# Kernel tuning notes

Measured on AMD Instinct MI355X. Metric: run time of the kernel, lower is better.

Reference implementation:

```python
import jax, jax.numpy as jnp
import numpy as np

RANKS = [16, 16, 16, 16]
ALPHAS = [32.0, 32.0, 32.0, 32.0]
IN_DIM, OUT_DIM = 4096, 4096
BSZ, SEQ = 4, 2048


def _col_scale(dtype):
    # per-column scale alpha_i / rank_i for each adapter's rank block
    s = np.concatenate([np.full(r, a / r, dtype=np.float32) for r, a in zip(RANKS, ALPHAS)])
    return jnp.asarray(s, dtype=dtype)


def setup_inputs() -> dict:
    key = jax.random.key(0)
    k1, k2, k3, k4 = jax.random.split(key, 4)
    total_rank = sum(RANKS)
    x = jax.random.normal(k1, (BSZ, SEQ, IN_DIM), dtype=jnp.float32)
    weight = jax.random.normal(k2, (OUT_DIM, IN_DIM), dtype=jnp.float32) * (1.0 / np.sqrt(IN_DIM))
    lora_a_weight = jax.random.normal(k3, (total_rank, IN_DIM), dtype=jnp.float32) * (1.0 / np.sqrt(IN_DIM))
    lora_b_weight = jax.random.normal(k4, (OUT_DIM, total_rank), dtype=jnp.float32) * 0.02
    return {"x": x, "weight": weight, "lora_a_weight": lora_a_weight, "lora_b_weight": lora_b_weight}


def reference(x, weight, lora_a_weight, lora_b_weight):
    # base: F.linear(x, W) -> x @ W^T        [B,S,out_dim]
    out = jnp.einsum('bsi,oi->bso', x, weight)
    # lora_a: x @ A^T                         [B,S,sum_rank] (dropout p=0 -> no-op)
    lora_a_out = jnp.einsum('bsi,ri->bsr', x, lora_a_weight)
    # The per-adapter masked loop sum_i (alpha_i/r_i) * (lora_a_out * mask_i) @ B^T
    # is mathematically a single GEMM with per-column scaling of lora_a_out.
    scaled = lora_a_out * _col_scale(lora_a_out.dtype)
    lora_out_total = jnp.einsum('bsr,or->bso', scaled, lora_b_weight)
    return out + lora_out_total
```

## Files before the change

kernel.cpp:

```cpp
#include <hip/hip_runtime.h>

typedef __bf16 bf16_t;
typedef __attribute__((ext_vector_type(8))) __bf16 bf16x8;
typedef __attribute__((ext_vector_type(4))) float f32x4;

#define M_DIM 8192
#define N_DIM 4096
#define K_DIM 4096
#define R_DIM 64

__global__ __launch_bounds__(256) void cvt_x(const float* __restrict__ in,
                                             bf16_t* __restrict__ out) {
    size_t i = ((size_t)blockIdx.x * 256 + threadIdx.x) * 8;
    float4 a = *(const float4*)(in + i);
    float4 b = *(const float4*)(in + i + 4);
    bf16x8 v;
    v[0] = (bf16_t)a.x; v[1] = (bf16_t)a.y; v[2] = (bf16_t)a.z; v[3] = (bf16_t)a.w;
    v[4] = (bf16_t)b.x; v[5] = (bf16_t)b.y; v[6] = (bf16_t)b.z; v[7] = (bf16_t)b.w;
    *(bf16x8*)(out + i) = v;
}

__global__ __launch_bounds__(256) void build_weff(const float* __restrict__ W,
                                                  const float* __restrict__ A,
                                                  const float* __restrict__ Bl,
                                                  bf16_t* __restrict__ out) {
    __shared__ __attribute__((aligned(16))) float bls[16 * R_DIM];

    const int i  = blockIdx.x * 256 + threadIdx.x;
    const int o0 = blockIdx.y * 16;

    {
        const int t = threadIdx.x;
        float4 v = *(const float4*)(Bl + o0 * R_DIM + t * 4);
        *(float4*)(bls + t * 4) = v;
    }
    __syncthreads();

    float acc[16];
#pragma unroll
    for (int j = 0; j < 16; j++) acc[j] = W[(size_t)(o0 + j) * K_DIM + i];

    for (int rh = 0; rh < R_DIM; rh += 16) {
        float av[16];
#pragma unroll
        for (int r = 0; r < 16; r++) av[r] = 2.0f * A[(size_t)(rh + r) * K_DIM + i];
#pragma unroll
        for (int j = 0; j < 16; j++) {
#pragma unroll
            for (int rq = 0; rq < 4; rq++) {
                float4 b = *(const float4*)(bls + j * R_DIM + rh + rq * 4);
                acc[j] = fmaf(b.x, av[rq * 4 + 0], acc[j]);
                acc[j] = fmaf(b.y, av[rq * 4 + 1], acc[j]);
                acc[j] = fmaf(b.z, av[rq * 4 + 2], acc[j]);
                acc[j] = fmaf(b.w, av[rq * 4 + 3], acc[j]);
            }
        }
    }
#pragma unroll
    for (int j = 0; j < 16; j++) out[(size_t)(o0 + j) * K_DIM + i] = (bf16_t)acc[j];
}

#define BM 256
#define BN 256
#define BK 64
#define NT (K_DIM / BK)

#define GLDS(gp, lp) __builtin_amdgcn_global_load_lds(                       \
    (__attribute__((address_space(1))) void*)(gp),                           \
    (__attribute__((address_space(3))) void*)(lp), 16, 0, 0)

#define SBAR() __builtin_amdgcn_s_barrier()
#define WAITV(n) asm volatile("s_waitcnt vmcnt(" #n ")" ::: "memory")

#define READ_A(ARR, mbase)                                                   \
    _Pragma("unroll")                                                        \
    for (int mf = 0; mf < 4; ++mf)                                           \
        afr[mf] = *(const bf16x8*)(&ARR[0][0] + aoff[(mbase) + mf]);

#define READ_B(ARR)                                                          \
    _Pragma("unroll")                                                        \
    for (int nf = 0; nf < 4; ++nf)                                           \
        bfr[nf] = *(const bf16x8*)(&ARR[0][0] + boff[nf]);

#define MFMA_HALF(mbase)                                                     \
    __builtin_amdgcn_s_setprio(1);                                           \
    _Pragma("unroll")                                                        \
    for (int mf = 0; mf < 4; ++mf)                                           \
        _Pragma("unroll")                                                    \
        for (int nf = 0; nf < 4; ++nf)                                       \
            acc[(mbase) + mf][nf] = __builtin_amdgcn_mfma_f32_16x16x32_bf16( \
                afr[mf], bfr[nf], acc[(mbase) + mf][nf], 0, 0, 0);           \
    __builtin_amdgcn_s_setprio(0);

#define STAGE(SRC, ROW0, KB, DST)                                            \
    _Pragma("unroll")                                                        \
    for (int j_ = 0; j_ < 2; ++j_) {                                         \
        const int g_  = wave * 2 + j_;                                       \
        const int r_  = g_ * 16 + srow;                                      \
        const int cs_ = sc ^ ((r_ >> 1) & 3);                                \
        GLDS(SRC + (size_t)((ROW0) + r_) * K_DIM + (KB) + cs_ * 8,           \
             &DST[0][0] + g_ * 512);                                         \
    }

#define KBODY(RA0, RA1, RB0, RB1, SA0, SA1, SB0, SB1, kn, pf)                \
    {                                                                        \
        bf16x8 afr[4], bfr[4];                                               \
                                   \
        READ_B(RB0); READ_A(RA0, 0);                                         \
        if (pf) { STAGE(Ax, m0, kn, SA0); }                                  \
        SBAR(); MFMA_HALF(0); SBAR();                                        \
         \
        READ_A(RA0, 4);                                                      \
        if (pf) { STAGE(Bw, n0, kn, SB0); }                                  \
        SBAR(); MFMA_HALF(4);                                                \
        if (pf) { WAITV(4); } else { WAITV(0); }                             \
        SBAR();                                                              \
                                   \
        READ_B(RB1); READ_A(RA1, 0);                                         \
        if (pf) { STAGE(Ax, m0, (kn) + 32, SA1); }                           \
        SBAR(); MFMA_HALF(0); SBAR();                                        \
        \
        READ_A(RA1, 4);                                                      \
        if (pf) { STAGE(Bw, n0, (kn) + 32, SB1); }                           \
        SBAR(); MFMA_HALF(4);                                                \
        if (pf) { WAITV(4); }                                                \
        SBAR();                                                              \
    }

__global__ __launch_bounds__(512, 2) void gemm_bf16(const bf16_t* __restrict__ Ax,
                                                    const bf16_t* __restrict__ Bw,
                                                    float* __restrict__ C) {
    __shared__ __attribute__((aligned(16))) bf16_t As0a[256][32], As0b[256][32];
    __shared__ __attribute__((aligned(16))) bf16_t As1a[256][32], As1b[256][32];
    __shared__ __attribute__((aligned(16))) bf16_t Bs0a[256][32], Bs0b[256][32];
    __shared__ __attribute__((aligned(16))) bf16_t Bs1a[256][32], Bs1b[256][32];

    const int tid  = threadIdx.x;
    const int wave = (tid >> 6) & 7;
    const int lane = tid & 63;
    const int m16  = lane & 15;
    const int quad = lane >> 4;
    const int wm   = wave >> 2;
    const int wn   = wave & 3;

    const int fid = blockIdx.y * 16 + blockIdx.x;
    const int swz = (fid & 7) * 64 + (fid >> 3);
    const int m0  = (swz >> 4) * BM;
    const int n0  = (swz & 15) * BN;

    const int srow = lane >> 2;
    const int sc   = lane & 3;

    int aoff[8], boff[4];
#pragma unroll
    for (int mf = 0; mf < 8; ++mf) {
        const int mr = wm * 128 + mf * 16 + m16;
        aoff[mf] = mr * 32 + ((quad ^ ((mr >> 1) & 3)) << 3);
    }
#pragma unroll
    for (int nf = 0; nf < 4; ++nf) {
        const int nr = wn * 64 + nf * 16 + m16;
        boff[nf] = nr * 32 + ((quad ^ ((nr >> 1) & 3)) << 3);
    }

    f32x4 acc[8][4] = {};

    STAGE(Ax, m0, 0,  As0a);
    STAGE(Bw, n0, 0,  Bs0a);
    STAGE(Ax, m0, 32, As0b);
    STAGE(Bw, n0, 32, Bs0b);
    WAITV(4);
    SBAR();

#pragma unroll 1
    for (int t = 0; t < NT; t += 2) {
        KBODY(As0a, As0b, Bs0a, Bs0b, As1a, As1b, Bs1a, Bs1b,
              (t + 1) * BK, true);
        const bool pf2 = (t + 2) < NT;
        KBODY(As1a, As1b, Bs1a, Bs1b, As0a, As0b, Bs0a, Bs0b,
              (t + 2) * BK, pf2);
    }

#pragma unroll
    for (int mf = 0; mf < 8; ++mf) {
#pragma unroll
        for (int i = 0; i < 4; ++i) {
            const int gm = m0 + wm * 128 + mf * 16 + quad * 4 + i;
            float* crow = C + (size_t)gm * N_DIM + n0 + wn * 64 + m16;
#pragma unroll
            for (int nf = 0; nf < 4; ++nf)
                crow[nf * 16] = acc[mf][nf][i];
        }
    }
}

extern "C" void kernel_launch(void* const* d_in, const int* in_sizes, int n_in,
                              void* d_out, int out_size, void* d_ws, size_t ws_size,
                              hipStream_t stream) {
    const float* x  = (const float*)d_in[0];
    const float* W  = (const float*)d_in[1];
    const float* La = (const float*)d_in[2];
    const float* Lb = (const float*)d_in[3];
    float* out = (float*)d_out;

    bf16_t* xb = (bf16_t*)d_ws;
    bf16_t* wf = (bf16_t*)((char*)d_ws + (size_t)M_DIM * K_DIM * sizeof(bf16_t));

    cvt_x<<<(M_DIM * K_DIM) / (256 * 8), 256, 0, stream>>>(x, xb);
    build_weff<<<dim3(K_DIM / 256, N_DIM / 16), 256, 0, stream>>>(W, La, Lb, wf);
    gemm_bf16<<<dim3(N_DIM / BN, M_DIM / BM), 512, 0, stream>>>(xb, wf, out);
}
```

Measured before the change: 606.6 us.

## Replace direct global-to-LDS loads with register-staged prefetch two tiles ahead

The GEMM main loop stops using global_load_lds DMA into shared memory. It now loads tiles into registers two K-steps ahead and writes them to swizzled LDS in the later MFMA halves, with an lgkmcnt wait before the barrier. The aim is deeper prefetch and latency hiding without explicit vmcnt waits. The cost is 16 extra bf16x8 registers per thread under launch_bounds(512,2), which risks spills or lower occupancy, and the LDS writes now go through VGPRs.

```diff
diff --git a/kernel.cpp b/kernel.cpp
--- a/kernel.cpp
+++ b/kernel.cpp
@@ -65,12 +65,8 @@
 #define BK 64
 #define NT (K_DIM / BK)
 
-#define GLDS(gp, lp) __builtin_amdgcn_global_load_lds(                       \
-    (__attribute__((address_space(1))) void*)(gp),                           \
-    (__attribute__((address_space(3))) void*)(lp), 16, 0, 0)
-
 #define SBAR() __builtin_amdgcn_s_barrier()
-#define WAITV(n) asm volatile("s_waitcnt vmcnt(" #n ")" ::: "memory")
+#define LGKM0() asm volatile("s_waitcnt lgkmcnt(0)" ::: "memory")
 
 #define READ_A(ARR, mbase)                                                   \
     _Pragma("unroll")                                                        \
@@ -92,38 +88,43 @@
                 afr[mf], bfr[nf], acc[(mbase) + mf][nf], 0, 0, 0);           \
     __builtin_amdgcn_s_setprio(0);
 
-#define STAGE(SRC, ROW0, KB, DST)                                            \
-    _Pragma("unroll")                                                        \
-    for (int j_ = 0; j_ < 2; ++j_) {                                         \
-        const int g_  = wave * 2 + j_;                                       \
-        const int r_  = g_ * 16 + srow;                                      \
-        const int cs_ = sc ^ ((r_ >> 1) & 3);                                \
-        GLDS(SRC + (size_t)((ROW0) + r_) * K_DIM + (KB) + cs_ * 8,           \
-             &DST[0][0] + g_ * 512);                                         \
-    }
-
-#define KBODY(RA0, RA1, RB0, RB1, SA0, SA1, SB0, SB1, kn, pf)                \
+#define ISSUE(R, P0, P1p, KI)                                                \
+    {                                                                        \
+        R[0] = *(const bf16x8*)((P0)  + (KI));                               \
+        R[1] = *(const bf16x8*)((P1p) + (KI));                               \
+        R[2] = *(const bf16x8*)((P0)  + (KI) + 32);                          \
+        R[3] = *(const bf16x8*)((P1p) + (KI) + 32);                          \
+    }
+
+#define WRITE(R, D0, D1)                                                     \
+    {                                                                        \
+        *(bf16x8*)(&D0[0][0] + w0) = R[0];                                   \
+        *(bf16x8*)(&D0[0][0] + w1) = R[1];                                   \
+        *(bf16x8*)(&D1[0][0] + w0) = R[2];                                   \
+        *(bf16x8*)(&D1[0][0] + w1) = R[3];                                   \
+    }
+
+#define KBODY(RA0, RA1, RB0, RB1, WA0, WA1, WB0, WB1, Wa, Wb, Ia, Ib, KI,    \
+              doI, doW)                                                      \
     {                                                                        \
         bf16x8 afr[4], bfr[4];                                               \
-                                   \
+                                                                     \
         READ_B(RB0); READ_A(RA0, 0);                                         \
-        if (pf) { STAGE(Ax, m0, kn, SA0); }                                  \
+        if (doI) { ISSUE(Ia, pA0, pA1, KI); }                                \
         SBAR(); MFMA_HALF(0); SBAR();                                        \
-         \
+                                                                     \
         READ_A(RA0, 4);                                                      \
-        if (pf) { STAGE(Bw, n0, kn, SB0); }                                  \
+        if (doI) { ISSUE(Ib, pB0, pB1, KI); }                                \
+        SBAR(); MFMA_HALF(4); SBAR();                                        \
+                                                                     \
+        READ_B(RB1); READ_A(RA1, 0);                                         \
+        SBAR(); MFMA_HALF(0);                                                \
+        if (doW) { WRITE(Wa, WA0, WA1); }                                    \
+        SBAR();                                                              \
+                                                                     \
+        READ_A(RA1, 4);                                                      \
         SBAR(); MFMA_HALF(4);                                                \
-        if (pf) { WAITV(4); } else { WAITV(0); }                             \
-        SBAR();                                                              \
-                                   \
-        READ_B(RB1); READ_A(RA1, 0);                                         \
-        if (pf) { STAGE(Ax, m0, (kn) + 32, SA1); }                           \
-        SBAR(); MFMA_HALF(0); SBAR();                                        \
-        \
-        READ_A(RA1, 4);                                                      \
-        if (pf) { STAGE(Bw, n0, (kn) + 32, SB1); }                           \
-        SBAR(); MFMA_HALF(4);                                                \
-        if (pf) { WAITV(4); }                                                \
+        if (doW) { WRITE(Wb, WB0, WB1); LGKM0(); }                           \
         SBAR();                                                              \
     }
 
@@ -150,6 +151,14 @@
 
     const int srow = lane >> 2;
     const int sc   = lane & 3;
+    const int r0   = wave * 32 + srow;
+    const int r1   = r0 + 16;
+    const bf16_t* pA0 = Ax + (size_t)(m0 + r0) * K_DIM + sc * 8;
+    const bf16_t* pA1 = Ax + (size_t)(m0 + r1) * K_DIM + sc * 8;
+    const bf16_t* pB0 = Bw + (size_t)(n0 + r0) * K_DIM + sc * 8;
+    const bf16_t* pB1 = Bw + (size_t)(n0 + r1) * K_DIM + sc * 8;
+    const int w0 = r0 * 32 + ((sc ^ ((r0 >> 1) & 3)) << 3);
+    const int w1 = r1 * 32 + ((sc ^ ((r1 >> 1) & 3)) << 3);
 
     int aoff[8], boff[4];
 #pragma unroll
@@ -164,21 +173,28 @@
     }
 
     f32x4 acc[8][4] = {};
-
-    STAGE(Ax, m0, 0,  As0a);
-    STAGE(Bw, n0, 0,  Bs0a);
-    STAGE(Ax, m0, 32, As0b);
-    STAGE(Bw, n0, 32, Bs0b);
-    WAITV(4);
+    bf16x8 rEa[4], rEb[4], rOa[4], rOb[4];
+
+    ISSUE(rEa, pA0, pA1, 0);
+    ISSUE(rEb, pB0, pB1, 0);
+    ISSUE(rOa, pA0, pA1, BK);
+    ISSUE(rOb, pB0, pB1, BK);
+    WRITE(rEa, As0a, As0b);
+    WRITE(rEb, Bs0a, Bs0b);
+    LGKM0();
     SBAR();
 
 #pragma unroll 1
     for (int t = 0; t < NT; t += 2) {
+        const int  ki_e = (t + 2) * BK;
+        const int  ki_o = (t + 3) * BK;
+        const bool di_e = (t + 2) < NT;
+        const bool di_o = (t + 3) < NT;
+        const bool dw_o = (t + 2) < NT;
         KBODY(As0a, As0b, Bs0a, Bs0b, As1a, As1b, Bs1a, Bs1b,
-              (t + 1) * BK, true);
-        const bool pf2 = (t + 2) < NT;
+              rOa, rOb, rEa, rEb, ki_e, di_e, true);
         KBODY(As1a, As1b, Bs1a, Bs1b, As0a, As0b, Bs0a, Bs0b,
-              (t + 2) * BK, pf2);
+              rEa, rEb, rOa, rOb, ki_o, di_o, dw_o);
     }
 
 #pragma unroll
```

Result: slower. 950.8 us (+56.8%).
